# Kernel tuning notes

Measured on AMD Instinct MI355X. Metric: run time of the kernel, lower is better.

The kernel has to match this reference:

```python
import jax, jax.numpy as jnp
import numpy as np

B, N, D_IN, D, H, L, NQ, NC, HID = 4, 25000, 32, 256, 8, 6, 100, 18, 1024


def _ln(x, g, b, eps=1e-5):
    m = jnp.mean(x, -1, keepdims=True)
    v = jnp.mean((x - m) ** 2, -1, keepdims=True)
    return (x - m) / jnp.sqrt(v + eps) * g + b


def _mha(q, kv, wqkv, bqkv, wo, bo, h):
    # q: (B, Lq, d), kv: (B, Lk, d); torch nn.MultiheadAttention math
    d = q.shape[-1]
    dh = d // h
    wq, wk, wv = jnp.split(wqkv, 3, axis=0)
    bq, bk, bv = jnp.split(bqkv, 3)
    Q = (q @ wq.T + bq).reshape(q.shape[0], q.shape[1], h, dh)
    K = (kv @ wk.T + bk).reshape(kv.shape[0], kv.shape[1], h, dh)
    V = (kv @ wv.T + bv).reshape(kv.shape[0], kv.shape[1], h, dh)
    s = jnp.einsum('bqhd,bkhd->bhqk', Q, K) / jnp.asarray(np.sqrt(dh), Q.dtype)
    a = jax.nn.softmax(s, axis=-1)
    o = jnp.einsum('bhqk,bkhd->bqhd', a, V).reshape(q.shape)
    return o @ wo.T + bo


def setup_inputs() -> dict:
    key = jax.random.key(0)
    ks = list(jax.random.split(key, 20))
    ki = iter(ks)

    def p(shape, s=0.02):
        return jax.random.normal(next(ki), shape, jnp.float32) * s

    inp = {
        'x': jax.random.normal(next(ki), (B * N, D_IN), jnp.float32),
        'batch_offsets': jnp.arange(B + 1, dtype=jnp.int32) * N,
        'ip_w': p((D, D_IN)), 'ip_b': jnp.zeros((D,), jnp.float32),
        'ip_ln_g': jnp.ones((D,), jnp.float32), 'ip_ln_b': jnp.zeros((D,), jnp.float32),
        'xm_w1': p((D, D_IN)), 'xm_b1': jnp.zeros((D,), jnp.float32),
        'xm_w2': p((D, D)), 'xm_b2': jnp.zeros((D,), jnp.float32),
        'query_embed': p((NQ, D), 1.0),
        'ca_wqkv': p((L, 3 * D, D)), 'ca_bqkv': jnp.zeros((L, 3 * D), jnp.float32),
        'ca_wo': p((L, D, D)), 'ca_bo': jnp.zeros((L, D), jnp.float32),
        'sa_wqkv': p((L, 3 * D, D)), 'sa_bqkv': jnp.zeros((L, 3 * D), jnp.float32),
        'sa_wo': p((L, D, D)), 'sa_bo': jnp.zeros((L, D), jnp.float32),
        'sa_ln_g': jnp.ones((L, D), jnp.float32), 'sa_ln_b': jnp.zeros((L, D), jnp.float32),
        'ffn_w1': p((L, HID, D)), 'ffn_b1': jnp.zeros((L, HID), jnp.float32),
        'ffn_w2': p((L, D, HID)), 'ffn_b2': jnp.zeros((L, D), jnp.float32),
        'ffn_ln_g': jnp.ones((L, D), jnp.float32), 'ffn_ln_b': jnp.zeros((L, D), jnp.float32),
        'out_ln_g': jnp.ones((D,), jnp.float32), 'out_ln_b': jnp.zeros((D,), jnp.float32),
        'cls_w1': p((D, D)), 'cls_b1': jnp.zeros((D,), jnp.float32),
        'cls_w2': p((NC + 1, D)), 'cls_b2': jnp.zeros((NC + 1,), jnp.float32),
    }
    return inp


def reference(x, batch_offsets, ip_w, ip_b, ip_ln_g, ip_ln_b, xm_w1, xm_b1, xm_w2, xm_b2,
              query_embed, ca_wqkv, ca_bqkv, ca_wo, ca_bo, sa_wqkv, sa_bqkv, sa_wo, sa_bo,
              sa_ln_g, sa_ln_b, ffn_w1, ffn_b1, ffn_w2, ffn_b2, ffn_ln_g, ffn_ln_b,
              out_ln_g, out_ln_b, cls_w1, cls_b1, cls_w2, cls_b2):
    b = batch_offsets.shape[0] - 1  # uniform segments -> batched attention
    n = x.shape[0] // b
    # input_proj: Linear -> LayerNorm -> ReLU
    inst = jax.nn.relu(_ln(x @ ip_w.T + ip_b, ip_ln_g, ip_ln_b)).reshape(b, n, -1)
    # x_mask: Linear -> ReLU -> Linear
    mask_feats = (jax.nn.relu(x @ xm_w1.T + xm_b1) @ xm_w2.T + xm_b2).reshape(b, n, -1)
    query = jnp.broadcast_to(query_embed, (b,) + query_embed.shape)
    for i in range(ca_wqkv.shape[0]):
        # CrossAttentionLayer: NOTE original discards dropout/norm results -> pure residual
        query = _mha(query, inst, ca_wqkv[i], ca_bqkv[i], ca_wo[i], ca_bo[i], H) + query
        # SelfAttentionLayer: residual + LayerNorm
        query = _ln(_mha(query, query, sa_wqkv[i], sa_bqkv[i], sa_wo[i], sa_bo[i], H) + query,
                    sa_ln_g[i], sa_ln_b[i])
        # FFN: residual + LayerNorm
        ff = jax.nn.relu(query @ ffn_w1[i].T + ffn_b1[i]) @ ffn_w2[i].T + ffn_b2[i]
        query = _ln(ff + query, ffn_ln_g[i], ffn_ln_b[i])
    qn = _ln(query, out_ln_g, out_ln_b)
    pred_labels = jax.nn.relu(qn @ cls_w1.T + cls_b1) @ cls_w2.T + cls_b2  # (b, NQ, NC+1)
    pred_masks = jnp.einsum('bqd,bnd->bqn', qn, mask_feats)  # (b, NQ, n)
    return pred_labels, pred_masks
```

## Files before the change

kernel.cpp:

```cpp
#include <hip/hip_runtime.h>

typedef unsigned short u16;
typedef unsigned int   u32;

constexpr int Bz   = 4;
constexpr int Ni   = 25000;
constexpr int BNi  = Bz * Ni;
constexpr int DIN  = 32;
constexpr int D    = 256;
constexpr int Hh   = 8;
constexpr int DH   = 32;
constexpr int Ll   = 6;
constexpr int NQ   = 100;
constexpr int NC1  = 19;
constexpr int HIDd = 1024;

constexpr int CHUNK  = 625;
constexpr int NCHUNK = Ni / CHUNK;
constexpr size_t PARTB = (size_t)Hh * NCHUNK * 128 * 34;
constexpr float SM_SCALE = 0.17677669529663687f;

__device__ __forceinline__ u16 f2b(float f) {
    union { float f; u32 u; } c; c.f = f;
    u32 u = c.u + 0x7FFFu + ((c.u >> 16) & 1u);
    return (u16)(u >> 16);
}

__global__ void k_cvt(const float* __restrict__ in, u16* __restrict__ out, int n) {
    for (int i = blockIdx.x * blockDim.x + threadIdx.x; i < n; i += gridDim.x * blockDim.x)
        out[i] = f2b(in[i]);
}

__device__ __forceinline__ void gload16(const u16* g, u16* l) {
    __builtin_amdgcn_global_load_lds(
        (const __attribute__((address_space(1))) void*)g,
        (__attribute__((address_space(3))) void*)l, 16, 0, 0);
}

typedef __attribute__((ext_vector_type(8))) __bf16 bf8v;
typedef __attribute__((ext_vector_type(8))) short  s8v;
typedef __attribute__((ext_vector_type(4))) float  f4v;

template<bool DOLN>
__global__ __launch_bounds__(512) void k_inproj(
    const float* __restrict__ x, int row0, int Mloc,
    const u16* __restrict__ w16, const float* __restrict__ bias,
    const float* __restrict__ g, const float* __restrict__ bb,
    u16* __restrict__ outb)
{
    __shared__ u16 Ws[256 * 40];
    __shared__ float Cb[256], Cg[256], Cbb[256];
    const int tid = threadIdx.x, lane = tid & 63, w = tid >> 6;
    const int lr = lane & 15, hi = lane >> 4;

    for (int ch = tid; ch < 1024; ch += 512) {
        int r = ch >> 2, g4 = ch & 3;
        *(uint4*)&Ws[r * 40 + g4 * 8] = *(const uint4*)(w16 + r * 32 + g4 * 8);
    }
    if (tid < 256) {
        Cb[tid] = bias[tid];
        if (DOLN) { Cg[tid] = g[tid]; Cbb[tid] = bb[tid]; }
    }

    const int rloc = blockIdx.x * 128 + w * 16 + lr;
    const int gr = row0 + min(rloc, Mloc - 1);
    bf8v xf;
    {
        const float* xp = x + (size_t)gr * DIN + hi * 8;
        float4 a = *(const float4*)xp, c = *(const float4*)(xp + 4);
        union { s8v s; bf8v b; } u;
        u.s[0] = (short)f2b(a.x); u.s[1] = (short)f2b(a.y);
        u.s[2] = (short)f2b(a.z); u.s[3] = (short)f2b(a.w);
        u.s[4] = (short)f2b(c.x); u.s[5] = (short)f2b(c.y);
        u.s[6] = (short)f2b(c.z); u.s[7] = (short)f2b(c.w);
        xf = u.b;
    }
    __syncthreads();

    f4v acc[16];
    #pragma unroll
    for (int ci = 0; ci < 16; ci++) {
        acc[ci] = (f4v){0.f, 0.f, 0.f, 0.f};
        bf8v af = *(const bf8v*)&Ws[(ci * 16 + lr) * 40 + hi * 8];
        acc[ci] = __builtin_amdgcn_mfma_f32_16x16x32_bf16(af, xf, acc[ci], 0, 0, 0);
    }
    #pragma unroll
    for (int ci = 0; ci < 16; ci++)
        #pragma unroll
        for (int r = 0; r < 4; r++)
            acc[ci][r] += Cb[ci * 16 + hi * 4 + r];

    float mean = 0.f, ri = 1.f;
    if (DOLN) {
        float s = 0.f, q = 0.f;
        #pragma unroll
        for (int ci = 0; ci < 16; ci++)
            #pragma unroll
            for (int r = 0; r < 4; r++) { s += acc[ci][r]; q += acc[ci][r] * acc[ci][r]; }
        s += __shfl_xor(s, 16); s += __shfl_xor(s, 32);
        q += __shfl_xor(q, 16); q += __shfl_xor(q, 32);
        mean = s * (1.f / D);
        float var = q * (1.f / D) - mean * mean;
        ri = rsqrtf(var + 1e-5f);
    }
    if (rloc < Mloc) {
        #pragma unroll
        for (int ci = 0; ci < 16; ci++) {
            u16 o[4];
            #pragma unroll
            for (int r = 0; r < 4; r++) {
                float v = acc[ci][r];
                if (DOLN) v = (v - mean) * ri * Cg[ci * 16 + hi * 4 + r] + Cbb[ci * 16 + hi * 4 + r];
                o[r] = f2b(fmaxf(v, 0.f));
            }
            uint2 pk;
            pk.x = (u32)o[0] | ((u32)o[1] << 16);
            pk.y = (u32)o[2] | ((u32)o[3] << 16);
            *(uint2*)&outb[(size_t)rloc * 256 + ci * 16 + hi * 4] = pk;
        }
    }
}

__global__ __launch_bounds__(256) void k_ln(
    const float* __restrict__ in, float* __restrict__ out,
    const float* __restrict__ g, const float* __restrict__ b)
{
    const int t = threadIdx.x;
    const int row = blockIdx.x;
    float v = in[(size_t)row * D + t];
    float s = v, q = v * v;
    #pragma unroll
    for (int off = 32; off >= 1; off >>= 1) { s += __shfl_xor(s, off); q += __shfl_xor(q, off); }
    __shared__ float red[2][4];
    const int wid = t >> 6;
    if ((t & 63) == 0) { red[0][wid] = s; red[1][wid] = q; }
    __syncthreads();
    float S = red[0][0] + red[0][1] + red[0][2] + red[0][3];
    float Q = red[1][0] + red[1][1] + red[1][2] + red[1][3];
    float m   = S * (1.f / D);
    float var = Q * (1.f / D) - m * m;
    float ri  = rsqrtf(var + 1e-5f);
    out[(size_t)row * D + t] = (v - m) * ri * g[t] + b[t];
}

__global__ __launch_bounds__(256) void k_bcast(const float* __restrict__ qe, float* __restrict__ q)
{
    const int t = threadIdx.x;
    const int r = blockIdx.x;
    q[(size_t)r * D + t] = qe[(size_t)(r % NQ) * D + t];
}

template<int BM, int BN, int TM, int TN>
__global__ __launch_bounds__(256) void k_gemm(
    const float* __restrict__ A, const float* __restrict__ W,
    const float* __restrict__ bias, const float* __restrict__ resid,
    float* __restrict__ C, int M, int N, int K, int relu)
{
    constexpr int BK = 16;
    constexpr int TX = BN / TN, TY = BM / TM;
    static_assert(TX * TY == 256, "block must be 256 threads");
    __shared__ float As[BK][BM + 4];
    __shared__ float Ws[BK][BN + 4];

    const int tid = threadIdx.x;
    const int tx = tid % TX, ty = tid / TX;
    const int row0 = blockIdx.y * BM, col0 = blockIdx.x * BN;

    float acc[TM][TN];
    #pragma unroll
    for (int i = 0; i < TM; i++)
        #pragma unroll
        for (int j = 0; j < TN; j++) acc[i][j] = 0.f;

    for (int k0 = 0; k0 < K; k0 += BK) {
        __syncthreads();
        for (int idx = tid; idx < BM * (BK / 4); idx += 256) {
            int r = idx / (BK / 4), c4 = idx % (BK / 4);
            int gr = row0 + r;
            float4 v;
            if (gr < M) v = *(const float4*)(A + (size_t)gr * K + k0 + c4 * 4);
            else { v.x = v.y = v.z = v.w = 0.f; }
            As[c4*4+0][r] = v.x; As[c4*4+1][r] = v.y; As[c4*4+2][r] = v.z; As[c4*4+3][r] = v.w;
        }
        for (int idx = tid; idx < BN * (BK / 4); idx += 256) {
            int n = idx / (BK / 4), c4 = idx % (BK / 4);
            int gn = col0 + n;
            float4 v;
            if (gn < N) v = *(const float4*)(W + (size_t)gn * K + k0 + c4 * 4);
            else { v.x = v.y = v.z = v.w = 0.f; }
            Ws[c4*4+0][n] = v.x; Ws[c4*4+1][n] = v.y; Ws[c4*4+2][n] = v.z; Ws[c4*4+3][n] = v.w;
        }
        __syncthreads();
        #pragma unroll
        for (int kk = 0; kk < BK; kk++) {
            float a[TM], bb[TN];
            #pragma unroll
            for (int i = 0; i < TM; i++) a[i] = As[kk][ty * TM + i];
            #pragma unroll
            for (int j = 0; j < TN; j++) bb[j] = Ws[kk][tx * TN + j];
            #pragma unroll
            for (int i = 0; i < TM; i++)
                #pragma unroll
                for (int j = 0; j < TN; j++)
                    acc[i][j] = fmaf(a[i], bb[j], acc[i][j]);
        }
    }

    #pragma unroll
    for (int i = 0; i < TM; i++) {
        int gr = row0 + ty * TM + i;
        if (gr >= M) continue;
        #pragma unroll
        for (int j = 0; j < TN; j++) {
            int gn = col0 + tx * TN + j;
            if (gn >= N) continue;
            float v = acc[i][j];
            if (bias)  v += bias[gn];
            if (resid) v += resid[(size_t)gr * N + gn];
            if (relu)  v = fmaxf(v, 0.f);
            C[(size_t)gr * N + gn] = v;
        }
    }
}

template<bool RELU>
__global__ __launch_bounds__(256) void mm_small(
    const float* __restrict__ A, const u16* __restrict__ W,
    const float* __restrict__ bias, const float* __restrict__ resid,
    float* __restrict__ C, int M, int N, int K)
{
    __shared__ u16 As[64 * 40];
    __shared__ u16 Bs[64 * 40];
    const int tid  = threadIdx.x;
    const int lane = tid & 63, w = tid >> 6;
    const int wm = w >> 1, wn = w & 1;
    const int row0 = blockIdx.y * 64, col0 = blockIdx.x * 64;
    const int lr = lane & 15, hi = lane >> 4;

    f4v acc[2][2];
    #pragma unroll
    for (int i = 0; i < 2; i++)
        #pragma unroll
        for (int j = 0; j < 2; j++) acc[i][j] = (f4v){0.f, 0.f, 0.f, 0.f};

    const int sr = tid >> 2, sc = (tid & 3) * 8;
    const int ga = min(row0 + sr, M - 1);
    const int gw = min(col0 + sr, N - 1);

    for (int k0 = 0; k0 < K; k0 += 32) {
        __syncthreads();
        {
            const float* ap = A + (size_t)ga * K + k0 + sc;
            float4 a = *(const float4*)ap, c = *(const float4*)(ap + 4);
            union { s8v s; uint4 u; } cv;
            cv.s[0] = (short)f2b(a.x); cv.s[1] = (short)f2b(a.y);
            cv.s[2] = (short)f2b(a.z); cv.s[3] = (short)f2b(a.w);
            cv.s[4] = (short)f2b(c.x); cv.s[5] = (short)f2b(c.y);
            cv.s[6] = (short)f2b(c.z); cv.s[7] = (short)f2b(c.w);
            *(uint4*)&As[sr * 40 + sc] = cv.u;
            *(uint4*)&Bs[sr * 40 + sc] = *(const uint4*)(W + (size_t)gw * K + k0 + sc);
        }
        __syncthreads();
        bf8v a0 = *(const bf8v*)&As[(wm * 32      + lr) * 40 + hi * 8];
        bf8v a1 = *(const bf8v*)&As[(wm * 32 + 16 + lr) * 40 + hi * 8];
        bf8v b0 = *(const bf8v*)&Bs[(wn * 32      + lr) * 40 + hi * 8];
        bf8v b1 = *(const bf8v*)&Bs[(wn * 32 + 16 + lr) * 40 + hi * 8];
        acc[0][0] = __builtin_amdgcn_mfma_f32_16x16x32_bf16(a0, b0, acc[0][0], 0, 0, 0);
        acc[0][1] = __builtin_amdgcn_mfma_f32_16x16x32_bf16(a0, b1, acc[0][1], 0, 0, 0);
        acc[1][0] = __builtin_amdgcn_mfma_f32_16x16x32_bf16(a1, b0, acc[1][0], 0, 0, 0);
        acc[1][1] = __builtin_amdgcn_mfma_f32_16x16x32_bf16(a1, b1, acc[1][1], 0, 0, 0);
    }

    const int crl = hi * 4, ccl = lr;
    #pragma unroll
    for (int mi = 0; mi < 2; mi++)
        #pragma unroll
        for (int ni = 0; ni < 2; ni++)
            #pragma unroll
            for (int r = 0; r < 4; r++) {
                int grow = row0 + wm * 32 + mi * 16 + crl + r;
                int gcol = col0 + wn * 32 + ni * 16 + ccl;
                if (grow < M && gcol < N) {
                    float v = acc[mi][ni][r];
                    if (bias)  v += bias[gcol];
                    if (resid) v += resid[(size_t)grow * N + gcol];
                    if (RELU)  v = fmaxf(v, 0.f);
                    C[(size_t)grow * N + gcol] = v;
                }
            }
}

template<bool OUTBF>
__global__ __launch_bounds__(256) void mm128(
    const u16* __restrict__ A, const u16* __restrict__ W,
    const float* __restrict__ bias, void* __restrict__ Cv,
    int M, int N, int K, long long sA, long long sW, long long sC)
{
    __shared__ u16 sm[8192];
    u16* As = sm;
    u16* Bs = sm + 4096;

    const int gx = gridDim.x, gy = gridDim.y;
    const int total = gx * gy * (int)gridDim.z;
    const int flat = blockIdx.x + gx * (blockIdx.y + gy * blockIdx.z);
    const int q8 = total >> 3, r8 = total & 7;
    const int xcd = flat & 7, blk = flat >> 3;
    const int swz = (xcd < r8 ? xcd * (q8 + 1) : r8 * (q8 + 1) + (xcd - r8) * q8) + blk;
    const int bx = swz % gx, by = (swz / gx) % gy, bz = swz / (gx * gy);

    A += (size_t)bz * sA;
    W += (size_t)bz * sW;
    const int tid = threadIdx.x, lane = tid & 63, w = tid >> 6;
    const int wm = w >> 1, wn = w & 1;
    const int row0 = by * 128, col0 = bx * 128;
    const int lr = lane & 15, hi = lane >> 4;
    const int srow = lane >> 2, scol = (lane & 3) * 8;

    f4v acc[4][4];
    #pragma unroll
    for (int i = 0; i < 4; i++)
        #pragma unroll
        for (int j = 0; j < 4; j++) acc[i][j] = (f4v){0.f, 0.f, 0.f, 0.f};

    for (int k0 = 0; k0 < K; k0 += 32) {
        __syncthreads();
        #pragma unroll
        for (int i = 0; i < 2; i++) {
            const int c = w * 2 + i;
            const int row = c * 16 + srow;
            const int gra = min(row0 + row, M - 1);
            const int grb = min(col0 + row, N - 1);
            gload16(A + (size_t)gra * K + k0 + scol, &As[c * 512]);
            gload16(W + (size_t)grb * K + k0 + scol, &Bs[c * 512]);
        }
        __syncthreads();
        bf8v a[4], bb[4];
        #pragma unroll
        for (int mi = 0; mi < 4; mi++)
            a[mi] = *(const bf8v*)&As[(wm * 64 + mi * 16 + lr) * 32 + hi * 8];
        #pragma unroll
        for (int ni = 0; ni < 4; ni++)
            bb[ni] = *(const bf8v*)&Bs[(wn * 64 + ni * 16 + lr) * 32 + hi * 8];
        #pragma unroll
        for (int mi = 0; mi < 4; mi++)
            #pragma unroll
            for (int ni = 0; ni < 4; ni++)
                acc[mi][ni] = __builtin_amdgcn_mfma_f32_16x16x32_bf16(a[mi], bb[ni], acc[mi][ni], 0, 0, 0);
    }

    if (OUTBF) {
        #pragma unroll
        for (int h0 = 0; h0 < 2; h0++) {
            __syncthreads();
            if (wm == h0) {
                #pragma unroll
                for (int mi = 0; mi < 4; mi++)
                    #pragma unroll
                    for (int ni = 0; ni < 4; ni++) {
                        int gcol = col0 + wn * 64 + ni * 16 + lr;
                        float bv = bias ? bias[gcol] : 0.f;
                        #pragma unroll
                        for (int r = 0; r < 4; r++) {
                            int lrow = mi * 16 + hi * 4 + r;
                            sm[lrow * 128 + wn * 64 + ni * 16 + lr] = f2b(acc[mi][ni][r] + bv);
                        }
                    }
            }
            __syncthreads();
            u16* Cb16 = (u16*)Cv + (size_t)bz * sC;
            #pragma unroll
            for (int j = 0; j < 4; j++) {
                int idx = tid + j * 256;
                int lrow = idx >> 4, c16 = idx & 15;
                int grow = row0 + h0 * 64 + lrow;
                if (grow < M)
                    *(uint4*)(Cb16 + (size_t)grow * N + col0 + c16 * 8) =
                        *(const uint4*)&sm[lrow * 128 + c16 * 8];
            }
        }
    } else {
        const int crl = hi * 4, ccl = lr;
        float* Cf = (float*)Cv + (size_t)bz * sC;
        #pragma unroll
        for (int mi = 0; mi < 4; mi++)
            #pragma unroll
            for (int ni = 0; ni < 4; ni++)
                #pragma unroll
                for (int r = 0; r < 4; r++) {
                    int grow = row0 + wm * 64 + mi * 16 + crl + r;
                    int gcol = col0 + wn * 64 + ni * 16 + ccl;
                    if (grow < M && gcol < N) {
                        float v = acc[mi][ni][r];
                        if (bias) v += bias[gcol];
                        Cf[(size_t)grow * N + gcol] = v;
                    }
                }
    }
}

__global__ __launch_bounds__(512) void k_flash(
    const float* __restrict__ qbuf, const u16* __restrict__ kv,
    float* __restrict__ part, int bBase, size_t kvStride, size_t pStride)
{
    const int tid = threadIdx.x;
    const int lane = tid & 63, w = tid >> 6;
    const int h = blockIdx.y;
    const int b = bBase + blockIdx.z;
    const u16* kvp = kv + (size_t)blockIdx.z * kvStride;
    float* pp = part + (size_t)blockIdx.z * pStride;
    const int k0loc = blockIdx.x * CHUNK;
    const int lr = lane & 15, hi = lane >> 4;

    __shared__ u16 Ks[64 * 40];
    __shared__ u16 Vt[32 * 72];
    __shared__ u16 Pt[8][16 * 72];

    const int qt = w * 16 + lr;
    const int qg = b * NQ + min(qt, NQ - 1);
    bf8v qf;
    {
        const float* Qp = qbuf + (size_t)qg * D + h * DH + hi * 8;
        union { s8v s; bf8v b; } qu;
        #pragma unroll
        for (int j = 0; j < 8; j++) qu.s[j] = (short)f2b(Qp[j] * SM_SCALE);
        qf = qu.b;
    }

    float m = -1e30f, l = 0.f;
    f4v o0 = (f4v){0.f,0.f,0.f,0.f}, o1 = (f4v){0.f,0.f,0.f,0.f};

    constexpr int NSTEP = (CHUNK + 63) / 64;
    for (int s = 0; s < NSTEP; s++) {
        const int ck = k0loc + s * 64;
        const int nv = min(64, k0loc + CHUNK - ck);
        __syncthreads();
        if (tid < 256) {
            int key = tid >> 2, g = tid & 3;
            int krow = min(ck + key, Ni - 1);
            *(uint4*)&Ks[key * 40 + g * 8] =
                *(const uint4*)(kvp + (size_t)krow * (2 * D) + h * DH + g * 8);
        } else {
            int t2 = tid - 256;
            int key = t2 >> 2, g = t2 & 3;
            int krow = min(ck + key, Ni - 1);
            uint4 u = *(const uint4*)(kvp + (size_t)krow * (2 * D) + D + h * DH + g * 8);
            const u16* pu = (const u16*)&u;
            #pragma unroll
            for (int j = 0; j < 8; j++) Vt[(g * 8 + j) * 72 + key] = pu[j];
        }
        __syncthreads();

        f4v sf[4];
        #pragma unroll
        for (int j = 0; j < 4; j++) {
            bf8v kf = *(const bf8v*)&Ks[(j * 16 + lr) * 40 + hi * 8];
            sf[j] = (f4v){0.f,0.f,0.f,0.f};
            sf[j] = __builtin_amdgcn_mfma_f32_16x16x32_bf16(kf, qf, sf[j], 0, 0, 0);
        }

        float sv[16];
        #pragma unroll
        for (int j = 0; j < 4; j++)
            #pragma unroll
            for (int r = 0; r < 4; r++) {
                int key0 = j * 16 + hi * 4 + r;
                sv[j * 4 + r] = (key0 < nv) ? sf[j][r] : -1e30f;
            }
        float smax = sv[0];
        #pragma unroll
        for (int j = 1; j < 16; j++) smax = fmaxf(smax, sv[j]);
        smax = fmaxf(smax, __shfl_xor(smax, 16));
        smax = fmaxf(smax, __shfl_xor(smax, 32));
        float mnew  = fmaxf(m, smax);
        float scale = __expf(m - mnew);
        m = mnew;

        float psum = 0.f;
        u16 pb[16];
        #pragma unroll
        for (int j = 0; j < 16; j++) {
            float p = __expf(sv[j] - mnew);
            psum += p;
            pb[j] = f2b(p);
        }
        psum += __shfl_xor(psum, 16);
        psum += __shfl_xor(psum, 32);
        l = l * scale + psum;

        u16* pw = &Pt[w][lr * 72];
        #pragma unroll
        for (int j = 0; j < 4; j++) {
            *(u32*)&pw[j * 16 + hi * 4]     = (u32)pb[j*4+0] | ((u32)pb[j*4+1] << 16);
            *(u32*)&pw[j * 16 + hi * 4 + 2] = (u32)pb[j*4+2] | ((u32)pb[j*4+3] << 16);
        }

        const int qb4 = hi * 4;
        float f0 = __shfl(scale, qb4 + 0);
        float f1 = __shfl(scale, qb4 + 1);
        float f2 = __shfl(scale, qb4 + 2);
        float f3 = __shfl(scale, qb4 + 3);
        o0[0] *= f0; o0[1] *= f1; o0[2] *= f2; o0[3] *= f3;
        o1[0] *= f0; o1[1] *= f1; o1[2] *= f2; o1[3] *= f3;

        #pragma unroll
        for (int j = 0; j < 2; j++) {
            bf8v pf  = *(const bf8v*)&Pt[w][lr * 72 + j * 32 + hi * 8];
            bf8v vf0 = *(const bf8v*)&Vt[lr * 72 + j * 32 + hi * 8];
            bf8v vf1 = *(const bf8v*)&Vt[(16 + lr) * 72 + j * 32 + hi * 8];
            o0 = __builtin_amdgcn_mfma_f32_16x16x32_bf16(pf, vf0, o0, 0, 0, 0);
            o1 = __builtin_amdgcn_mfma_f32_16x16x32_bf16(pf, vf1, o1, 0, 0, 0);
        }
    }

    const size_t pbase = ((size_t)(h * NCHUNK + blockIdx.x) * 128) * 34;
    #pragma unroll
    for (int r = 0; r < 4; r++) {
        int qtr = w * 16 + hi * 4 + r;
        pp[pbase + (size_t)qtr * 34 + 2 + lr]      = o0[r];
        pp[pbase + (size_t)qtr * 34 + 2 + 16 + lr] = o1[r];
    }
    if (lane < 16) {
        pp[pbase + (size_t)(w * 16 + lane) * 34 + 0] = m;
        pp[pbase + (size_t)(w * 16 + lane) * 34 + 1] = l;
    }
}

__global__ __launch_bounds__(64) void k_fmerge(const float* __restrict__ part,
                                               float* __restrict__ abuf, int bBase, size_t pStride)
{
    const float* pz = part + (size_t)blockIdx.y * pStride;
    const int b = bBase + blockIdx.y;
    const int t = threadIdx.x;
    const int hq = blockIdx.x;
    const int h = hq / NQ, q = hq % NQ;
    float mmax = -1e30f;
    for (int c = 0; c < NCHUNK; c++)
        mmax = fmaxf(mmax, pz[((size_t)(h * NCHUNK + c) * 128 + q) * 34]);
    float L = 0.f, a = 0.f;
    for (int c = 0; c < NCHUNK; c++) {
        const float* p = &pz[((size_t)(h * NCHUNK + c) * 128 + q) * 34];
        float wv = __expf(p[0] - mmax);
        L += wv * p[1];
        if (t < DH) a += wv * p[2 + t];
    }
    if (t < DH)
        abuf[((size_t)(b * NQ + q)) * D + h * DH + t] = a / L;
}

__global__ __launch_bounds__(128) void k_sattn(const float* __restrict__ sqkv, float* __restrict__ abuf)
{
    const int tid = threadIdx.x;
    const int bh = blockIdx.x;
    const int b = bh >> 3, h = bh & 7;
    __shared__ float Ks[NQ][DH], Vs[NQ][DH];
    for (int idx = tid; idx < NQ * 8; idx += 128) {
        int kk = idx >> 3, f4 = idx & 7;
        const float* base = sqkv + ((size_t)(b * NQ + kk)) * (3 * D) + h * DH;
        *(float4*)&Ks[kk][f4 * 4] = *(const float4*)(base + D + f4 * 4);
        *(float4*)&Vs[kk][f4 * 4] = *(const float4*)(base + 2 * D + f4 * 4);
    }
    float qr[DH];
    const int q = tid;
    if (q < NQ) {
        const float* Qp = sqkv + ((size_t)(b * NQ + q)) * (3 * D) + h * DH;
        #pragma unroll
        for (int d = 0; d < DH; d += 4) {
            float4 v = *(const float4*)(Qp + d);
            qr[d] = v.x * SM_SCALE; qr[d+1] = v.y * SM_SCALE;
            qr[d+2] = v.z * SM_SCALE; qr[d+3] = v.w * SM_SCALE;
        }
    } else {
        #pragma unroll
        for (int d = 0; d < DH; d++) qr[d] = 0.f;
    }
    __syncthreads();
    float m = -1e30f, l = 0.f, acc[DH];
    #pragma unroll
    for (int d = 0; d < DH; d++) acc[d] = 0.f;
    for (int kk = 0; kk < NQ; kk++) {
        float sc = 0.f;
        #pragma unroll
        for (int d = 0; d < DH; d++) sc += qr[d] * Ks[kk][d];
        if (sc > m) {
            float r = __expf(m - sc);
            l *= r;
            #pragma unroll
            for (int d = 0; d < DH; d++) acc[d] *= r;
            m = sc;
        }
        float p = __expf(sc - m);
        l += p;
        #pragma unroll
        for (int d = 0; d < DH; d++) acc[d] += p * Vs[kk][d];
    }
    if (q < NQ) {
        float li = 1.f / l;
        float* o = abuf + ((size_t)(b * NQ + q)) * D + h * DH;
        #pragma unroll
        for (int d = 0; d < DH; d++) o[d] = acc[d] * li;
    }
}

extern "C" void kernel_launch(void* const* d_in, const int* in_sizes, int n_in,
                              void* d_out, int out_size, void* d_ws, size_t ws_size,
                              hipStream_t stream)
{
    const float* x        = (const float*)d_in[0];
    const float* ip_w     = (const float*)d_in[2];
    const float* ip_b     = (const float*)d_in[3];
    const float* ip_g     = (const float*)d_in[4];
    const float* ip_bb    = (const float*)d_in[5];
    const float* xm_w1    = (const float*)d_in[6];
    const float* xm_b1    = (const float*)d_in[7];
    const float* xm_w2    = (const float*)d_in[8];
    const float* xm_b2    = (const float*)d_in[9];
    const float* qe       = (const float*)d_in[10];
    const float* ca_wqkv  = (const float*)d_in[11];
    const float* ca_bqkv  = (const float*)d_in[12];
    const float* ca_wo    = (const float*)d_in[13];
    const float* ca_bo    = (const float*)d_in[14];
    const float* sa_wqkv  = (const float*)d_in[15];
    const float* sa_bqkv  = (const float*)d_in[16];
    const float* sa_wo    = (const float*)d_in[17];
    const float* sa_bo    = (const float*)d_in[18];
    const float* sa_ln_g  = (const float*)d_in[19];
    const float* sa_ln_b  = (const float*)d_in[20];
    const float* ffn_w1   = (const float*)d_in[21];
    const float* ffn_b1   = (const float*)d_in[22];
    const float* ffn_w2   = (const float*)d_in[23];
    const float* ffn_b2   = (const float*)d_in[24];
    const float* ffn_ln_g = (const float*)d_in[25];
    const float* ffn_ln_b = (const float*)d_in[26];
    const float* out_ln_g = (const float*)d_in[27];
    const float* out_ln_b = (const float*)d_in[28];
    const float* cls_w1   = (const float*)d_in[29];
    const float* cls_b1   = (const float*)d_in[30];
    const float* cls_w2   = (const float*)d_in[31];
    const float* cls_b2   = (const float*)d_in[32];
    float* out = (float*)d_out;

    bool batched = false;
    int instRows;
    if      (ws_size >= 210000000ull) { batched = true; instRows = BNi; }
    else if (ws_size >= 112000000ull) { instRows = BNi; }
    else if (ws_size >=  73000000ull) { instRows = Ni;  }
    else return;
    const bool instFull = (instRows == BNi);
    const int nzb = batched ? Bz : 1;

    char* wp = (char*)d_ws;
    auto alloc = [&](size_t bytes) -> char* {
        char* r = wp; wp += (bytes + 255) & ~(size_t)255; return r;
    };
    u16*   instb = (u16*)  alloc((size_t)instRows * D * 2);
    u16*   kvb   = (u16*)  alloc((size_t)(batched ? BNi : Ni) * 2 * D * 2);
    float* part  = (float*)alloc((size_t)nzb * PARTB * 4);
    float* qbuf  = (float*)alloc(409600);
    float* abuf  = (float*)alloc(409600);
    float* sqkv  = (float*)alloc(1228800);
    float* f1b   = (float*)alloc(1638400);
    float* qA    = (float*)alloc(409600);
    float* qB    = (float*)alloc(409600);
    u16*   ipw16 = (u16*)  alloc(256 * 32 * 2);
    u16*   xw116 = (u16*)  alloc(256 * 32 * 2);
    u16*   xw216 = (u16*)  alloc((size_t)D * D * 2);
    u16*   caq16 = (u16*)  alloc((size_t)Ll * 3 * D * D * 2);
    u16*   saq16 = (u16*)  alloc((size_t)Ll * 3 * D * D * 2);
    u16*   cao16 = (u16*)  alloc((size_t)Ll * D * D * 2);
    u16*   sao16 = (u16*)  alloc((size_t)Ll * D * D * 2);
    u16*   fw116 = (u16*)  alloc((size_t)Ll * HIDd * D * 2);
    u16*   fw216 = (u16*)  alloc((size_t)Ll * D * HIDd * 2);
    u16*   qnb   = (u16*)  alloc((size_t)Bz * NQ * D * 2);

    k_cvt<<<16,   256, 0, stream>>>(ip_w,  ipw16, 256 * 32);
    k_cvt<<<16,   256, 0, stream>>>(xm_w1, xw116, 256 * 32);
    k_cvt<<<64,   256, 0, stream>>>(xm_w2, xw216, D * D);
    k_cvt<<<1024, 256, 0, stream>>>(ca_wqkv, caq16, Ll * 3 * D * D);
    k_cvt<<<1024, 256, 0, stream>>>(sa_wqkv, saq16, Ll * 3 * D * D);
    k_cvt<<<512,  256, 0, stream>>>(ca_wo, cao16, Ll * D * D);
    k_cvt<<<512,  256, 0, stream>>>(sa_wo, sao16, Ll * D * D);
    k_cvt<<<1024, 256, 0, stream>>>(ffn_w1, fw116, Ll * HIDd * D);
    k_cvt<<<1024, 256, 0, stream>>>(ffn_w2, fw216, Ll * D * HIDd);

    if (instFull)
        k_inproj<true><<<(BNi + 127) / 128, 512, 0, stream>>>(
            x, 0, BNi, ipw16, ip_b, ip_g, ip_bb, instb);
    k_bcast<<<Bz * NQ, 256, 0, stream>>>(qe, qA);

    float* qcur = qA;
    float* qtmp = qB;
    for (int i = 0; i < Ll; i++) {
        const u16*   wq16  = caq16 + (size_t)i * 3 * D * D;
        const u16*   wkv16 = wq16 + (size_t)D * D;
        const float* bqkv  = ca_bqkv + (size_t)i * 3 * D;
        mm_small<false><<<dim3(4, 7), 256, 0, stream>>>(
            qcur, wq16, bqkv, nullptr, qbuf, Bz * NQ, D, D);
        if (batched) {
            mm128<true><<<dim3(4, 196, 4), 256, 0, stream>>>(
                instb, wkv16, bqkv + D, kvb, Ni, 2 * D, D,
                (long long)Ni * D, 0, (long long)Ni * 2 * D);
            k_flash<<<dim3(NCHUNK, Hh, 4), 512, 0, stream>>>(
                qbuf, kvb, part, 0, (size_t)Ni * 2 * D, PARTB);
            k_fmerge<<<dim3(Hh * NQ, 4), 64, 0, stream>>>(part, abuf, 0, PARTB);
        } else {
            for (int b = 0; b < Bz; b++) {
                if (!instFull)
                    k_inproj<true><<<(Ni + 127) / 128, 512, 0, stream>>>(
                        x, b * Ni, Ni, ipw16, ip_b, ip_g, ip_bb, instb);
                const u16* ip = instFull ? instb + (size_t)b * Ni * D : instb;
                mm128<true><<<dim3(4, 196, 1), 256, 0, stream>>>(
                    ip, wkv16, bqkv + D, kvb, Ni, 2 * D, D, 0, 0, 0);
                k_flash<<<dim3(NCHUNK, Hh, 1), 512, 0, stream>>>(
                    qbuf, kvb, part, b, 0, 0);
                k_fmerge<<<dim3(Hh * NQ, 1), 64, 0, stream>>>(part, abuf, b, 0);
            }
        }
        mm_small<false><<<dim3(4, 7), 256, 0, stream>>>(
            abuf, cao16 + (size_t)i * D * D, ca_bo + (size_t)i * D, qcur, qtmp,
            Bz * NQ, D, D);
        { float* t2 = qcur; qcur = qtmp; qtmp = t2; }
        mm_small<false><<<dim3(12, 7), 256, 0, stream>>>(
            qcur, saq16 + (size_t)i * 3 * D * D, sa_bqkv + (size_t)i * 3 * D, nullptr, sqkv,
            Bz * NQ, 3 * D, D);
        k_sattn<<<Bz * Hh, 128, 0, stream>>>(sqkv, abuf);
        mm_small<false><<<dim3(4, 7), 256, 0, stream>>>(
            abuf, sao16 + (size_t)i * D * D, sa_bo + (size_t)i * D, qcur, qtmp,
            Bz * NQ, D, D);
        k_ln<<<Bz * NQ, 256, 0, stream>>>(qtmp, qtmp, sa_ln_g + i * D, sa_ln_b + i * D);
        { float* t2 = qcur; qcur = qtmp; qtmp = t2; }
        mm_small<true><<<dim3(16, 7), 256, 0, stream>>>(
            qcur, fw116 + (size_t)i * HIDd * D, ffn_b1 + (size_t)i * HIDd, nullptr, f1b,
            Bz * NQ, HIDd, D);
        mm_small<false><<<dim3(4, 7), 256, 0, stream>>>(
            f1b, fw216 + (size_t)i * D * HIDd, ffn_b2 + (size_t)i * D, qcur, qtmp,
            Bz * NQ, D, HIDd);
        k_ln<<<Bz * NQ, 256, 0, stream>>>(qtmp, qtmp, ffn_ln_g + i * D, ffn_ln_b + i * D);
        { float* t2 = qcur; qcur = qtmp; qtmp = t2; }
    }

    float* qn = qbuf;
    k_ln<<<Bz * NQ, 256, 0, stream>>>(qcur, qn, out_ln_g, out_ln_b);
    k_gemm<64,64,4,4><<<dim3(4, 7), 256, 0, stream>>>(
        qn, cls_w1, cls_b1, nullptr, abuf, Bz * NQ, D, D, 1);
    k_gemm<64,64,4,4><<<dim3(1, 7), 256, 0, stream>>>(
        abuf, cls_w2, cls_b2, nullptr, out, Bz * NQ, NC1, D, 0);

    k_cvt<<<128, 256, 0, stream>>>(qn, qnb, Bz * NQ * D);
    if (instFull) {
        k_inproj<false><<<(BNi + 127) / 128, 512, 0, stream>>>(
            x, 0, BNi, xw116, xm_b1, nullptr, nullptr, instb);
        if (batched) {
            mm128<true><<<dim3(2, 196, 4), 256, 0, stream>>>(
                instb, xw216, xm_b2, kvb, Ni, D, D,
                (long long)Ni * D, 0, (long long)Ni * D);
            mm128<false><<<dim3(196, 1, 4), 256, 0, stream>>>(
                qnb, kvb, nullptr, out + Bz * NQ * NC1, NQ, Ni, D,
                (long long)NQ * D, (long long)Ni * D, (long long)NQ * Ni);
        } else {
            for (int b = 0; b < Bz; b++) {
                mm128<true><<<dim3(2, 196, 1), 256, 0, stream>>>(
                    instb + (size_t)b * Ni * D, xw216, xm_b2, kvb, Ni, D, D, 0, 0, 0);
                mm128<false><<<dim3(196, 1, 1), 256, 0, stream>>>(
                    qnb + (size_t)b * NQ * D, kvb, nullptr,
                    out + Bz * NQ * NC1 + (size_t)b * NQ * Ni, NQ, Ni, D, 0, 0, 0);
            }
        }
    } else {
        for (int b = 0; b < Bz; b++) {
            k_inproj<false><<<(Ni + 127) / 128, 512, 0, stream>>>(
                x, b * Ni, Ni, xw116, xm_b1, nullptr, nullptr, instb);
            mm128<true><<<dim3(2, 196, 1), 256, 0, stream>>>(
                instb, xw216, xm_b2, kvb, Ni, D, D, 0, 0, 0);
            mm128<false><<<dim3(196, 1, 1), 256, 0, stream>>>(
                qnb + (size_t)b * NQ * D, kvb, nullptr,
                out + Bz * NQ * NC1 + (size_t)b * NQ * Ni, NQ, Ni, D, 0, 0, 0);
        }
    }
}
```

Measured before the change: 1.782 ms.

## Batch cross-attention K/V projections across layers and use hardware bf16 conversion

Measured after the change: 1.731 ms. 1.03x faster.

```diff
diff --git a/kernel.cpp b/kernel.cpp
--- a/kernel.cpp
+++ b/kernel.cpp
@@ -21,9 +21,10 @@
 constexpr float SM_SCALE = 0.17677669529663687f;
 
 __device__ __forceinline__ u16 f2b(float f) {
-    union { float f; u32 u; } c; c.f = f;
-    u32 u = c.u + 0x7FFFu + ((c.u >> 16) & 1u);
-    return (u16)(u >> 16);
+    union { __bf16 h; u16 u; } c; c.h = (__bf16)f; return c.u;
+}
+__device__ __forceinline__ u32 pk2(float a, float b) {
+    union { __bf16 h[2]; u32 u; } c; c.h[0] = (__bf16)a; c.h[1] = (__bf16)b; return c.u;
 }
 
 __global__ void k_cvt(const float* __restrict__ in, u16* __restrict__ out, int n) {
@@ -106,17 +107,17 @@
     if (rloc < Mloc) {
         #pragma unroll
         for (int ci = 0; ci < 16; ci++) {
-            u16 o[4];
+            float v0[4];
             #pragma unroll
             for (int r = 0; r < 4; r++) {
                 float v = acc[ci][r];
                 if (DOLN) v = (v - mean) * ri * Cg[ci * 16 + hi * 4 + r] + Cbb[ci * 16 + hi * 4 + r];
-                o[r] = f2b(fmaxf(v, 0.f));
+                v0[r] = fmaxf(v, 0.f);
             }
-            uint2 pk;
-            pk.x = (u32)o[0] | ((u32)o[1] << 16);
-            pk.y = (u32)o[2] | ((u32)o[3] << 16);
-            *(uint2*)&outb[(size_t)rloc * 256 + ci * 16 + hi * 4] = pk;
+            uint2 pkv;
+            pkv.x = pk2(v0[0], v0[1]);
+            pkv.y = pk2(v0[2], v0[3]);
+            *(uint2*)&outb[(size_t)rloc * 256 + ci * 16 + hi * 4] = pkv;
         }
     }
 }
@@ -252,12 +253,10 @@
         {
             const float* ap = A + (size_t)ga * K + k0 + sc;
             float4 a = *(const float4*)ap, c = *(const float4*)(ap + 4);
-            union { s8v s; uint4 u; } cv;
-            cv.s[0] = (short)f2b(a.x); cv.s[1] = (short)f2b(a.y);
-            cv.s[2] = (short)f2b(a.z); cv.s[3] = (short)f2b(a.w);
-            cv.s[4] = (short)f2b(c.x); cv.s[5] = (short)f2b(c.y);
-            cv.s[6] = (short)f2b(c.z); cv.s[7] = (short)f2b(c.w);
-            *(uint4*)&As[sr * 40 + sc] = cv.u;
+            uint4 u;
+            u.x = pk2(a.x, a.y); u.y = pk2(a.z, a.w);
+            u.z = pk2(c.x, c.y); u.w = pk2(c.z, c.w);
+            *(uint4*)&As[sr * 40 + sc] = u;
             *(uint4*)&Bs[sr * 40 + sc] = *(const uint4*)(W + (size_t)gw * K + k0 + sc);
         }
         __syncthreads();
@@ -294,7 +293,8 @@
 __global__ __launch_bounds__(256) void mm128(
     const u16* __restrict__ A, const u16* __restrict__ W,
     const float* __restrict__ bias, void* __restrict__ Cv,
-    int M, int N, int K, long long sA, long long sW, long long sC)
+    int M, int N, int K, long long sA, long long sW, long long sC,
+    int zmod, long long sW2, long long sBias)
 {
     __shared__ u16 sm[8192];
     u16* As = sm;
@@ -308,8 +308,10 @@
     const int swz = (xcd < r8 ? xcd * (q8 + 1) : r8 * (q8 + 1) + (xcd - r8) * q8) + blk;
     const int bx = swz % gx, by = (swz / gx) % gy, bz = swz / (gx * gy);
 
-    A += (size_t)bz * sA;
-    W += (size_t)bz * sW;
+    const int aidx = bz % zmod, widx = bz / zmod;
+    A += (size_t)aidx * sA;
+    W += (size_t)aidx * sW + (size_t)widx * sW2;
+    if (bias) bias += (size_t)widx * sBias;
     const int tid = threadIdx.x, lane = tid & 63, w = tid >> 6;
     const int wm = w >> 1, wn = w & 1;
     const int row0 = by * 128, col0 = bx * 128;
@@ -475,13 +477,12 @@
         float scale = __expf(m - mnew);
         m = mnew;
 
+        float pv[16];
         float psum = 0.f;
-        u16 pb[16];
         #pragma unroll
         for (int j = 0; j < 16; j++) {
-            float p = __expf(sv[j] - mnew);
-            psum += p;
-            pb[j] = f2b(p);
+            pv[j] = __expf(sv[j] - mnew);
+            psum += pv[j];
         }
         psum += __shfl_xor(psum, 16);
         psum += __shfl_xor(psum, 32);
@@ -490,8 +491,8 @@
         u16* pw = &Pt[w][lr * 72];
         #pragma unroll
         for (int j = 0; j < 4; j++) {
-            *(u32*)&pw[j * 16 + hi * 4]     = (u32)pb[j*4+0] | ((u32)pb[j*4+1] << 16);
-            *(u32*)&pw[j * 16 + hi * 4 + 2] = (u32)pb[j*4+2] | ((u32)pb[j*4+3] << 16);
+            *(u32*)&pw[j * 16 + hi * 4]     = pk2(pv[j*4+0], pv[j*4+1]);
+            *(u32*)&pw[j * 16 + hi * 4 + 2] = pk2(pv[j*4+2], pv[j*4+3]);
         }
 
         const int qb4 = hi * 4;
@@ -640,8 +641,11 @@
     float* out = (float*)d_out;
 
     bool batched = false;
+    int kvG = 1;
     int instRows;
-    if      (ws_size >= 210000000ull) { batched = true; instRows = BNi; }
+    if      (ws_size >= 740000000ull) { batched = true; kvG = 6; instRows = BNi; }
+    else if (ws_size >= 430000000ull) { batched = true; kvG = 3; instRows = BNi; }
+    else if (ws_size >= 210000000ull) { batched = true; kvG = 1; instRows = BNi; }
     else if (ws_size >= 112000000ull) { instRows = BNi; }
     else if (ws_size >=  73000000ull) { instRows = Ni;  }
     else return;
@@ -653,7 +657,7 @@
         char* r = wp; wp += (bytes + 255) & ~(size_t)255; return r;
     };
     u16*   instb = (u16*)  alloc((size_t)instRows * D * 2);
-    u16*   kvb   = (u16*)  alloc((size_t)(batched ? BNi : Ni) * 2 * D * 2);
+    u16*   kvb   = (u16*)  alloc((batched ? (size_t)kvG * Bz * Ni * 2 * D : (size_t)Ni * 2 * D) * 2);
     float* part  = (float*)alloc((size_t)nzb * PARTB * 4);
     float* qbuf  = (float*)alloc(409600);
     float* abuf  = (float*)alloc(409600);
@@ -689,32 +693,8 @@
 
     float* qcur = qA;
     float* qtmp = qB;
-    for (int i = 0; i < Ll; i++) {
-        const u16*   wq16  = caq16 + (size_t)i * 3 * D * D;
-        const u16*   wkv16 = wq16 + (size_t)D * D;
-        const float* bqkv  = ca_bqkv + (size_t)i * 3 * D;
-        mm_small<false><<<dim3(4, 7), 256, 0, stream>>>(
-            qcur, wq16, bqkv, nullptr, qbuf, Bz * NQ, D, D);
-        if (batched) {
-            mm128<true><<<dim3(4, 196, 4), 256, 0, stream>>>(
-                instb, wkv16, bqkv + D, kvb, Ni, 2 * D, D,
-                (long long)Ni * D, 0, (long long)Ni * 2 * D);
-            k_flash<<<dim3(NCHUNK, Hh, 4), 512, 0, stream>>>(
-                qbuf, kvb, part, 0, (size_t)Ni * 2 * D, PARTB);
-            k_fmerge<<<dim3(Hh * NQ, 4), 64, 0, stream>>>(part, abuf, 0, PARTB);
-        } else {
-            for (int b = 0; b < Bz; b++) {
-                if (!instFull)
-                    k_inproj<true><<<(Ni + 127) / 128, 512, 0, stream>>>(
-                        x, b * Ni, Ni, ipw16, ip_b, ip_g, ip_bb, instb);
-                const u16* ip = instFull ? instb + (size_t)b * Ni * D : instb;
-                mm128<true><<<dim3(4, 196, 1), 256, 0, stream>>>(
-                    ip, wkv16, bqkv + D, kvb, Ni, 2 * D, D, 0, 0, 0);
-                k_flash<<<dim3(NCHUNK, Hh, 1), 512, 0, stream>>>(
-                    qbuf, kvb, part, b, 0, 0);
-                k_fmerge<<<dim3(Hh * NQ, 1), 64, 0, stream>>>(part, abuf, b, 0);
-            }
-        }
+
+    auto layer_tail = [&](int i) {
         mm_small<false><<<dim3(4, 7), 256, 0, stream>>>(
             abuf, cao16 + (size_t)i * D * D, ca_bo + (size_t)i * D, qcur, qtmp,
             Bz * NQ, D, D);
@@ -736,6 +716,47 @@
             Bz * NQ, D, HIDd);
         k_ln<<<Bz * NQ, 256, 0, stream>>>(qtmp, qtmp, ffn_ln_g + i * D, ffn_ln_b + i * D);
         { float* t2 = qcur; qcur = qtmp; qtmp = t2; }
+    };
+
+    if (batched) {
+        for (int l0 = 0; l0 < Ll; l0 += kvG) {
+            mm128<true><<<dim3(4, 196, 4 * kvG), 256, 0, stream>>>(
+                instb, caq16 + (size_t)l0 * 3 * D * D + (size_t)D * D,
+                ca_bqkv + (size_t)l0 * 3 * D + D, kvb, Ni, 2 * D, D,
+                (long long)Ni * D, 0, (long long)Ni * 2 * D,
+                4, (long long)3 * D * D, (long long)3 * D);
+            for (int i = l0; i < l0 + kvG; i++) {
+                const u16* wq16 = caq16 + (size_t)i * 3 * D * D;
+                const float* bqkv = ca_bqkv + (size_t)i * 3 * D;
+                mm_small<false><<<dim3(4, 7), 256, 0, stream>>>(
+                    qcur, wq16, bqkv, nullptr, qbuf, Bz * NQ, D, D);
+                const u16* kvl = kvb + (size_t)(i - l0) * Bz * Ni * 2 * D;
+                k_flash<<<dim3(NCHUNK, Hh, 4), 512, 0, stream>>>(
+                    qbuf, kvl, part, 0, (size_t)Ni * 2 * D, PARTB);
+                k_fmerge<<<dim3(Hh * NQ, 4), 64, 0, stream>>>(part, abuf, 0, PARTB);
+                layer_tail(i);
+            }
+        }
+    } else {
+        for (int i = 0; i < Ll; i++) {
+            const u16* wq16  = caq16 + (size_t)i * 3 * D * D;
+            const u16* wkv16 = wq16 + (size_t)D * D;
+            const float* bqkv = ca_bqkv + (size_t)i * 3 * D;
+            mm_small<false><<<dim3(4, 7), 256, 0, stream>>>(
+                qcur, wq16, bqkv, nullptr, qbuf, Bz * NQ, D, D);
+            for (int b = 0; b < Bz; b++) {
+                if (!instFull)
+                    k_inproj<true><<<(Ni + 127) / 128, 512, 0, stream>>>(
+                        x, b * Ni, Ni, ipw16, ip_b, ip_g, ip_bb, instb);
+                const u16* ip = instFull ? instb + (size_t)b * Ni * D : instb;
+                mm128<true><<<dim3(4, 196, 1), 256, 0, stream>>>(
+                    ip, wkv16, bqkv + D, kvb, Ni, 2 * D, D, 0, 0, 0, 4, 0, 0);
+                k_flash<<<dim3(NCHUNK, Hh, 1), 512, 0, stream>>>(
+                    qbuf, kvb, part, b, 0, 0);
+                k_fmerge<<<dim3(Hh * NQ, 1), 64, 0, stream>>>(part, abuf, b, 0);
+            }
+            layer_tail(i);
+        }
     }
 
     float* qn = qbuf;
@@ -752,17 +773,17 @@
         if (batched) {
             mm128<true><<<dim3(2, 196, 4), 256, 0, stream>>>(
                 instb, xw216, xm_b2, kvb, Ni, D, D,
-                (long long)Ni * D, 0, (long long)Ni * D);
+                (long long)Ni * D, 0, (long long)Ni * D, 4, 0, 0);
             mm128<false><<<dim3(196, 1, 4), 256, 0, stream>>>(
                 qnb, kvb, nullptr, out + Bz * NQ * NC1, NQ, Ni, D,
-                (long long)NQ * D, (long long)Ni * D, (long long)NQ * Ni);
+                (long long)NQ * D, (long long)Ni * D, (long long)NQ * Ni, 4, 0, 0);
         } else {
             for (int b = 0; b < Bz; b++) {
                 mm128<true><<<dim3(2, 196, 1), 256, 0, stream>>>(
-                    instb + (size_t)b * Ni * D, xw216, xm_b2, kvb, Ni, D, D, 0, 0, 0);
+                    instb + (size_t)b * Ni * D, xw216, xm_b2, kvb, Ni, D, D, 0, 0, 0, 4, 0, 0);
                 mm128<false><<<dim3(196, 1, 1), 256, 0, stream>>>(
                     qnb + (size_t)b * NQ * D, kvb, nullptr,
-                    out + Bz * NQ * NC1 + (size_t)b * NQ * Ni, NQ, Ni, D, 0, 0, 0);
+                    out + Bz * NQ * NC1 + (size_t)b * NQ * Ni, NQ, Ni, D, 0, 0, 0, 4, 0, 0);
             }
         }
     } else {
@@ -770,10 +791,10 @@
             k_inproj<false><<<(Ni + 127) / 128, 512, 0, stream>>>(
                 x, b * Ni, Ni, xw116, xm_b1, nullptr, nullptr, instb);
             mm128<true><<<dim3(2, 196, 1), 256, 0, stream>>>(
-                instb, xw216, xm_b2, kvb, Ni, D, D, 0, 0, 0);
+                instb, xw216, xm_b2, kvb, Ni, D, D, 0, 0, 0, 4, 0, 0);
             mm128<false><<<dim3(196, 1, 1), 256, 0, stream>>>(
                 qnb + (size_t)b * NQ * D, kvb, nullptr,
-                out + Bz * NQ * NC1 + (size_t)b * NQ * Ni, NQ, Ni, D, 0, 0, 0);
-        }
-    }
-}
+                out + Bz * NQ * NC1 + (size_t)b * NQ * Ni, NQ, Ni, D, 0, 0, 0, 4, 0, 0);
+        }
+    }
+}
```
